# Kernel tuning notes

Hardware: AMD Instinct MI355X
Metric: run time of the kernel (lower is better)

The kernel has to match this reference:

```python
import jax, jax.numpy as jnp
import numpy as np

DIM = 2560; HEADS = 20; HEAD_DIM = 128
N_EXP = 4; TOP_K = 2; HID = 6912; SHID = 3584
B = 1; S = 2048
EPS = 1e-6


def setup_inputs():
    key = jax.random.key(0)
    ks = jax.random.split(key, 16)
    r = lambda i, shape, s=0.02: jax.random.normal(ks[i], shape, jnp.float32) * s
    # rope as [1,S,1,HD/2,2,2] rotation matrices: [[cos,-sin],[sin,cos]]
    ang = jax.random.uniform(ks[0], (1, S, 1, HEAD_DIM // 2), jnp.float32) * (2.0 * np.pi)
    c, s_ = jnp.cos(ang), jnp.sin(ang)
    rope = jnp.stack([jnp.stack([c, -s_], -1), jnp.stack([s_, c], -1)], -2)
    return dict(
        hidden_states=jax.random.normal(ks[1], (B, S, DIM), jnp.float32),
        temb=jax.random.normal(ks[2], (B, DIM), jnp.float32),
        rope=rope,
        adaln_w=r(3, (6 * DIM, DIM)), adaln_b=jnp.zeros((6 * DIM,), jnp.float32),
        qkv_w=r(4, (3 * DIM, DIM)), qkv_b=jnp.zeros((3 * DIM,), jnp.float32),
        qn_w=jnp.ones((DIM,), jnp.float32), kn_w=jnp.ones((DIM,), jnp.float32),
        out_w=r(5, (DIM, DIM)), out_b=jnp.zeros((DIM,), jnp.float32),
        gate_w=r(6, (N_EXP, DIM), 1.0 / DIM ** 0.5),
        ew1=r(7, (N_EXP, HID, DIM)), ew2=r(8, (N_EXP, DIM, HID)), ew3=r(9, (N_EXP, HID, DIM)),
        sw1=r(10, (SHID, DIM)), sw2=r(11, (DIM, SHID)), sw3=r(12, (SHID, DIM)),
    )


def _layernorm(x):  # elementwise_affine=False, eps=1e-6
    m = x.mean(-1, keepdims=True)
    v = ((x - m) ** 2).mean(-1, keepdims=True)
    return (x - m) * jax.lax.rsqrt(v + EPS)


def _rmsnorm(x, w):  # DistributedRMSNorm, tp_size=1
    return x * jax.lax.rsqrt((x ** 2).mean(-1, keepdims=True) + EPS) * w


def _apply_rope(x, rope):  # x:[B,S,H,D], rope:[1,S,1,D/2,2,2]
    b, s, h, d = x.shape
    x_ = x.reshape(b, s, h, d // 2, 1, 2)
    out = rope[..., 0] * x_[..., 0] + rope[..., 1] * x_[..., 1]  # [B,S,H,D/2,2]
    return out.reshape(b, s, h, d)


def _swiglu(x, w1, w2, w3):
    return (jax.nn.silu(x @ w1.T) * (x @ w3.T)) @ w2.T


def _forward(hidden_states, temb, rope, adaln_w, adaln_b, qkv_w, qkv_b, qn_w, kn_w,
             out_w, out_b, gate_w, ew1, ew2, ew3, sw1, sw2, sw3):
    b, s, d = hidden_states.shape
    # adaLN modulation: SiLU -> Linear -> [:, None] -> chunk(6)
    mod = (jax.nn.silu(temb) @ adaln_w.T + adaln_b)[:, None, :]
    shift_msa, scale_msa, gate_msa, shift_mlp, scale_mlp, gate_mlp = jnp.split(mod, 6, axis=-1)
    # --- attention ---
    nh = _layernorm(hidden_states) * (1.0 + scale_msa) + shift_msa
    qkv = nh @ qkv_w.T + qkv_b
    q, k, v = jnp.split(qkv, 3, axis=-1)  # each [B,S,inner_dim]
    q = _rmsnorm(q, qn_w)  # RMS over full inner_dim (all heads)
    k = _rmsnorm(k, kn_w)
    q = q.reshape(b, s, HEADS, HEAD_DIM)
    k = k.reshape(b, s, HEADS, HEAD_DIM)
    v = v.reshape(b, s, HEADS, HEAD_DIM)
    q = _apply_rope(q, rope)
    k = _apply_rope(k, rope)
    attn = jnp.einsum('bqhd,bkhd->bhqk', q, k) * (HEAD_DIM ** -0.5)
    attn = jax.nn.softmax(attn, axis=-1)
    o = jnp.einsum('bhqk,bkhd->bqhd', attn, v).reshape(b, s, HEADS * HEAD_DIM)
    o = o @ out_w.T + out_b
    hidden_states = gate_msa * o + hidden_states
    # --- MoE SwiGLU feed-forward ---
    nh = _layernorm(hidden_states) * (1.0 + scale_mlp) + shift_mlp
    x = nh.reshape(-1, d)  # [T,d]
    scores = jax.nn.softmax(x @ gate_w.T, axis=-1)  # [T,E]
    tw, ti = jax.lax.top_k(scores, TOP_K)  # norm_topk_prob=False
    t = x.shape[0]
    wdense = jnp.zeros((t, N_EXP), x.dtype).at[jnp.arange(t)[:, None], ti].set(tw)
    y = jnp.zeros_like(x)
    for e in range(N_EXP):  # fixed small expert count
        y = y + wdense[:, e:e + 1] * _swiglu(x, ew1[e], ew2[e], ew3[e])
    y = y.reshape(b, s, d) + _swiglu(nh, sw1, sw2, sw3)  # shared experts on identity
    return gate_mlp * y + hidden_states


def reference(hidden_states, temb, rope, adaln_w, adaln_b, qkv_w, qkv_b, qn_w, kn_w,
              out_w, out_b, gate_w, ew1, ew2, ew3, sw1, sw2, sw3):
    return _forward(hidden_states, temb, rope, adaln_w, adaln_b, qkv_w, qkv_b, qn_w, kn_w,
                    out_w, out_b, gate_w, ew1, ew2, ew3, sw1, sw2, sw3)
```

## Files before the change

### kernel.cpp

```cpp
#include <hip/hip_runtime.h>

#define DIM 2560
#define T_TOK 2048
#define NHEADS 20
#define HD 128
#define HID_E 6912
#define SHID_E 3584
#define MPAD 5120

typedef _Float16 f16x8 __attribute__((ext_vector_type(8)));
typedef float f32x4 __attribute__((ext_vector_type(4)));
typedef unsigned short u16x8 __attribute__((ext_vector_type(8)));

#define MFMA16(a, b, c) __builtin_amdgcn_mfma_f32_16x16x32_f16((a), (b), (c), 0, 0, 0)

__device__ inline unsigned short f2h(float f) {
  return __builtin_bit_cast(unsigned short, (_Float16)f);
}
__device__ inline float h2f(unsigned short u) {
  return (float)__builtin_bit_cast(_Float16, u);
}
__device__ inline float wave_sum(float v) {
#pragma unroll
  for (int off = 32; off > 0; off >>= 1) v += __shfl_down(v, off, 64);
  return v;
}
__device__ inline void gld16(const void* g, void* l) {
  __builtin_amdgcn_global_load_lds((const __attribute__((address_space(1))) void*)g,
                                   (__attribute__((address_space(3))) void*)l, 16, 0, 0);
}


__global__ __launch_bounds__(256) void silu_k(const float* __restrict__ t,
                                              float* __restrict__ ss) {
  int i = blockIdx.x * 256 + threadIdx.x;
  if (i < DIM) {
    float v = t[i];
    ss[i] = v / (1.f + expf(-v));
  }
}

__global__ __launch_bounds__(256) void cvt_f16(const float* __restrict__ in,
                                               unsigned short* __restrict__ outp, int n8) {
  const int stride = gridDim.x * 256;
  for (int i = blockIdx.x * 256 + threadIdx.x; i < n8; i += stride) {
    float4 a = *(const float4*)(in + (size_t)i * 8);
    float4 b = *(const float4*)(in + (size_t)i * 8 + 4);
    u16x8 u;
    u[0] = f2h(a.x); u[1] = f2h(a.y); u[2] = f2h(a.z); u[3] = f2h(a.w);
    u[4] = f2h(b.x); u[5] = f2h(b.y); u[6] = f2h(b.z); u[7] = f2h(b.w);
    *(u16x8*)&outp[(size_t)i * 8] = u;
  }
}

__global__ __launch_bounds__(256) void cvt_pair(const float* __restrict__ w1,
                                                const float* __restrict__ w3,
                                                unsigned short* __restrict__ outp) {
  const int j = blockIdx.x;
  const int g = j >> 5, r = j & 31;
  const float* src = (r < 16) ? (w1 + (size_t)(g * 16 + r) * DIM)
                              : (w3 + (size_t)(g * 16 + (r & 15)) * DIM);
  unsigned short* dst = outp + (size_t)j * DIM;
  for (int i = threadIdx.x; i < 320; i += 256) {
    float4 a = *(const float4*)(src + i * 8);
    float4 b = *(const float4*)(src + i * 8 + 4);
    u16x8 u;
    u[0] = f2h(a.x); u[1] = f2h(a.y); u[2] = f2h(a.z); u[3] = f2h(a.w);
    u[4] = f2h(b.x); u[5] = f2h(b.y); u[6] = f2h(b.z); u[7] = f2h(b.w);
    *(u16x8*)&dst[i * 8] = u;
  }
}

__global__ __launch_bounds__(256) void adaln_gemv(const float* __restrict__ ss,
                                                  const float* __restrict__ W,
                                                  const float* __restrict__ bias,
                                                  float* __restrict__ mod) {
  const int lane = threadIdx.x & 63;
  const int j = blockIdx.x * 4 + (threadIdx.x >> 6);
  const float* wr = W + (size_t)j * DIM;
  float p = 0.f;
  for (int i = lane; i < 640; i += 64) {
    float4 w = *(const float4*)(wr + i * 4);
    float4 x = *(const float4*)(ss + i * 4);
    p += w.x * x.x + w.y * x.y + w.z * x.z + w.w * x.w;
  }
  p = wave_sum(p);
  if (lane == 0) mod[j] = p + bias[j];
}

__global__ __launch_bounds__(256) void ln_mod(const float* __restrict__ x,
                                              const float* __restrict__ shift,
                                              const float* __restrict__ scale,
                                              unsigned short* __restrict__ outp) {
  __shared__ float rbuf[8];
  const int t = blockIdx.x, tid = threadIdx.x, lane = tid & 63, wid = tid >> 6;
  const float* xr = x + (size_t)t * DIM;
  float s = 0.f, sq = 0.f;
  for (int i = tid; i < 640; i += 256) {
    float4 v = *(const float4*)(xr + i * 4);
    s += v.x + v.y + v.z + v.w;
    sq += v.x * v.x + v.y * v.y + v.z * v.z + v.w * v.w;
  }
  s = wave_sum(s);
  sq = wave_sum(sq);
  if (lane == 0) {
    rbuf[wid] = s;
    rbuf[4 + wid] = sq;
  }
  __syncthreads();
  float S = rbuf[0] + rbuf[1] + rbuf[2] + rbuf[3];
  float SQ = rbuf[4] + rbuf[5] + rbuf[6] + rbuf[7];
  float mean = S * (1.f / DIM);
  float rs = rsqrtf(SQ * (1.f / DIM) - mean * mean + 1e-6f);
  for (int i = tid; i < 640; i += 256) {
    float4 v = *(const float4*)(xr + i * 4);
    float4 sc4 = *(const float4*)(scale + i * 4);
    float4 sh4 = *(const float4*)(shift + i * 4);
    ushort4 u;
    u.x = f2h((v.x - mean) * rs * (1.f + sc4.x) + sh4.x);
    u.y = f2h((v.y - mean) * rs * (1.f + sc4.y) + sh4.y);
    u.z = f2h((v.z - mean) * rs * (1.f + sc4.z) + sh4.z);
    u.w = f2h((v.w - mean) * rs * (1.f + sc4.w) + sh4.w);
    *(ushort4*)&outp[(size_t)t * DIM + i * 4] = u;
  }
}

__global__ __launch_bounds__(256) void rmsrope(const unsigned short* __restrict__ qkv,
                                               const float* __restrict__ qn,
                                               const float* __restrict__ kn,
                                               const float* __restrict__ rope,
                                               unsigned short* __restrict__ qh,
                                               unsigned short* __restrict__ kh) {
  __shared__ float rbuf[8];
  const int t = blockIdx.x, tid = threadIdx.x, lane = tid & 63, wid = tid >> 6;
  const unsigned short* row = qkv + (size_t)t * 7680;
  float sq = 0.f, sk = 0.f;
  for (int i = tid; i < 320; i += 256) {
    f16x8 qv = *(const f16x8*)(row + i * 8);
    f16x8 kv = *(const f16x8*)(row + DIM + i * 8);
#pragma unroll
    for (int j = 0; j < 8; ++j) {
      float q = (float)qv[j], k = (float)kv[j];
      sq += q * q;
      sk += k * k;
    }
  }
  sq = wave_sum(sq);
  sk = wave_sum(sk);
  if (lane == 0) {
    rbuf[wid] = sq;
    rbuf[4 + wid] = sk;
  }
  __syncthreads();
  float SQ = rbuf[0] + rbuf[1] + rbuf[2] + rbuf[3];
  float SK = rbuf[4] + rbuf[5] + rbuf[6] + rbuf[7];
  float rq = rsqrtf(SQ * (1.f / DIM) + 1e-6f) * 0.08838834764831845f;
  float rk = rsqrtf(SK * (1.f / DIM) + 1e-6f);
  for (int pp = tid; pp < 1280; pp += 256) {
    int c = pp * 2;
    float qe = h2f(row[c]) * rq * qn[c], qo = h2f(row[c + 1]) * rq * qn[c + 1];
    float ke = h2f(row[DIM + c]) * rk * kn[c], ko = h2f(row[DIM + c + 1]) * rk * kn[c + 1];
    float4 rr = *(const float4*)(rope + (size_t)t * 256 + (pp & 63) * 4);
    unsigned qp = (unsigned)f2h(rr.x * qe + rr.y * qo) |
                  ((unsigned)f2h(rr.z * qe + rr.w * qo) << 16);
    unsigned kp = (unsigned)f2h(rr.x * ke + rr.y * ko) |
                  ((unsigned)f2h(rr.z * ke + rr.w * ko) << 16);
    *(unsigned*)&qh[(size_t)t * DIM + c] = qp;
    *(unsigned*)&kh[(size_t)t * DIM + c] = kp;
  }
}

__global__ void transpose_v(const unsigned short* __restrict__ in,
                            unsigned short* __restrict__ outp) {
  __shared__ unsigned short tile[32][33];
  const int bx = blockIdx.x * 32;
  const int by = blockIdx.y * 32;
  const int tx = threadIdx.x, ty = threadIdx.y;
  for (int j = ty; j < 32; j += 8)
    tile[j][tx] = in[(size_t)(by + j) * 7680 + 5120 + bx + tx];
  __syncthreads();
  for (int j = ty; j < 32; j += 8)
    outp[(size_t)(bx + j) * T_TOK + by + tx] = tile[tx][j];
}

__global__ __launch_bounds__(256) void fattn(const unsigned short* __restrict__ qh,
                                             const unsigned short* __restrict__ kh,
                                             const unsigned short* __restrict__ vt,
                                             unsigned short* __restrict__ obuf) {
  __shared__ unsigned short sK[64 * 128];
  __shared__ unsigned short sV[128 * 64];
  __shared__ unsigned short sP[64 * 64];
  __shared__ float sRedM[4][64];
  __shared__ float sRedL[4][64];
  __shared__ float sM[64];
  __shared__ float sL[64];
  const int tid = threadIdx.x, lane = tid & 63, wv = tid >> 6;
  const int g = lane >> 4, fr = lane & 15;
  const int h = blockIdx.y;
  const int q0 = blockIdx.x * 64;

  {
    const int r = tid >> 2, qt = tid & 3;
    const unsigned short* gp = qh + (size_t)(q0 + r) * DIM + h * HD + qt * 32;
    uint4 v0 = ((const uint4*)gp)[0];
    uint4 v1 = ((const uint4*)gp)[1];
    uint4 v2 = ((const uint4*)gp)[2];
    uint4 v3 = ((const uint4*)gp)[3];
    unsigned short* dst = &sK[r * 128];
    const int cb = qt * 4, rs = r & 15;
    *(uint4*)&dst[((cb + 0) ^ rs) * 8] = v0;
    *(uint4*)&dst[((cb + 1) ^ rs) * 8] = v1;
    *(uint4*)&dst[((cb + 2) ^ rs) * 8] = v2;
    *(uint4*)&dst[((cb + 3) ^ rs) * 8] = v3;
  }
  __syncthreads();
  f16x8 qfrag[4][4];
#pragma unroll
  for (int ni = 0; ni < 4; ++ni) {
#pragma unroll
    for (int kt = 0; kt < 4; ++kt) {
      int r = ni * 16 + fr;
      qfrag[ni][kt] = *(const f16x8*)&sK[r * 128 + (((kt * 4 + g) ^ (r & 15)) << 3)];
    }
  }
  __syncthreads();

  f32x4 acco[4][2];
  f32x4 mprev[4];
  float mrun[4], lrun[4];
#pragma unroll
  for (int i = 0; i < 4; ++i) {
    acco[i][0] = (f32x4)0.f;
    acco[i][1] = (f32x4)0.f;
    mprev[i] = (f32x4)(-1e30f);
    mrun[i] = -1e30f;
    lrun[i] = 0.f;
  }

  for (int kt0 = 0; kt0 < T_TOK; kt0 += 64) {
    {
      const int r = tid >> 2, qt = tid & 3;
      const unsigned short* gp = kh + (size_t)(kt0 + r) * DIM + h * HD + qt * 32;
      uint4 v0 = ((const uint4*)gp)[0];
      uint4 v1 = ((const uint4*)gp)[1];
      uint4 v2 = ((const uint4*)gp)[2];
      uint4 v3 = ((const uint4*)gp)[3];
      unsigned short* dst = &sK[r * 128];
      const int cb = qt * 4, rs = r & 15;
      *(uint4*)&dst[((cb + 0) ^ rs) * 8] = v0;
      *(uint4*)&dst[((cb + 1) ^ rs) * 8] = v1;
      *(uint4*)&dst[((cb + 2) ^ rs) * 8] = v2;
      *(uint4*)&dst[((cb + 3) ^ rs) * 8] = v3;
      const int rv = tid >> 1, hf = tid & 1;
      const unsigned short* gv = vt + (size_t)(h * HD + rv) * T_TOK + kt0 + hf * 32;
      uint4 w0 = ((const uint4*)gv)[0];
      uint4 w1 = ((const uint4*)gv)[1];
      uint4 w2 = ((const uint4*)gv)[2];
      uint4 w3 = ((const uint4*)gv)[3];
      unsigned short* dv = &sV[rv * 64];
      const int cv = hf * 4, rvs = rv & 7;
      *(uint4*)&dv[((cv + 0) ^ rvs) * 8] = w0;
      *(uint4*)&dv[((cv + 1) ^ rvs) * 8] = w1;
      *(uint4*)&dv[((cv + 2) ^ rvs) * 8] = w2;
      *(uint4*)&dv[((cv + 3) ^ rvs) * 8] = w3;
    }
    __syncthreads();

    f32x4 accs[4] = {(f32x4)0.f, (f32x4)0.f, (f32x4)0.f, (f32x4)0.f};
#pragma unroll
    for (int kt = 0; kt < 4; ++kt) {
      int r = wv * 16 + fr;
      f16x8 ak = *(const f16x8*)&sK[r * 128 + (((kt * 4 + g) ^ (r & 15)) << 3)];
#pragma unroll
      for (int ni = 0; ni < 4; ++ni) accs[ni] = MFMA16(ak, qfrag[ni][kt], accs[ni]);
    }

    float pm[4];
#pragma unroll
    for (int ni = 0; ni < 4; ++ni) {
      float m = fmaxf(fmaxf(accs[ni][0], accs[ni][1]), fmaxf(accs[ni][2], accs[ni][3]));
      m = fmaxf(m, __shfl_xor(m, 16));
      m = fmaxf(m, __shfl_xor(m, 32));
      pm[ni] = m;
    }
    if (g == 0) {
#pragma unroll
      for (int ni = 0; ni < 4; ++ni) sRedM[wv][ni * 16 + fr] = pm[ni];
    }
    __syncthreads();
    float mnew[4];
#pragma unroll
    for (int ni = 0; ni < 4; ++ni) {
      int q = ni * 16 + fr;
      float mt = fmaxf(fmaxf(sRedM[0][q], sRedM[1][q]), fmaxf(sRedM[2][q], sRedM[3][q]));
      mnew[ni] = fmaxf(mrun[ni], mt);
    }
    float lsum[4];
#pragma unroll
    for (int ni = 0; ni < 4; ++ni) {
      float l0 = 0.f;
#pragma unroll
      for (int i = 0; i < 4; ++i) {
        float p = __expf(accs[ni][i] - mnew[ni]);
        accs[ni][i] = p;
        l0 += p;
      }
      l0 += __shfl_xor(l0, 16);
      l0 += __shfl_xor(l0, 32);
      lsum[ni] = l0;
    }
    if (g == 0) {
#pragma unroll
      for (int ni = 0; ni < 4; ++ni) sRedL[wv][ni * 16 + fr] = lsum[ni];
      if (wv == 0) {
#pragma unroll
        for (int ni = 0; ni < 4; ++ni) sM[ni * 16 + fr] = mnew[ni];
      }
    }
#pragma unroll
    for (int ni = 0; ni < 4; ++ni) {
      int q = ni * 16 + fr;
      unsigned p01 = (unsigned)f2h(accs[ni][0]) | ((unsigned)f2h(accs[ni][1]) << 16);
      unsigned p23 = (unsigned)f2h(accs[ni][2]) | ((unsigned)f2h(accs[ni][3]) << 16);
      uint2 pk;
      pk.x = p01;
      pk.y = p23;
      *(uint2*)&sP[q * 64 + ((((wv << 1) | (g >> 1)) ^ (q & 7)) << 3) + ((g & 1) << 2)] = pk;
    }
    __syncthreads();
#pragma unroll
    for (int ni = 0; ni < 4; ++ni) {
      int q = ni * 16 + fr;
      float lt = sRedL[0][q] + sRedL[1][q] + sRedL[2][q] + sRedL[3][q];
      lrun[ni] = lrun[ni] * __expf(mrun[ni] - mnew[ni]) + lt;
      mrun[ni] = mnew[ni];
    }

#pragma unroll
    for (int mi = 0; mi < 4; ++mi) {
      f32x4 mn = *(const f32x4*)&sM[mi * 16 + g * 4];
      f32x4 sc;
#pragma unroll
      for (int i = 0; i < 4; ++i) sc[i] = __expf(mprev[mi][i] - mn[i]);
      acco[mi][0] *= sc;
      acco[mi][1] *= sc;
      mprev[mi] = mn;
    }
#pragma unroll
    for (int ktp = 0; ktp < 2; ++ktp) {
      f16x8 bv[2];
#pragma unroll
      for (int nd = 0; nd < 2; ++nd) {
        int r = wv * 32 + nd * 16 + fr;
        bv[nd] = *(const f16x8*)&sV[r * 64 + (((ktp * 4 + g) ^ (r & 7)) << 3)];
      }
#pragma unroll
      for (int mi = 0; mi < 4; ++mi) {
        int r = mi * 16 + fr;
        f16x8 ap = *(const f16x8*)&sP[r * 64 + (((ktp * 4 + g) ^ (r & 7)) << 3)];
        acco[mi][0] = MFMA16(ap, bv[0], acco[mi][0]);
        acco[mi][1] = MFMA16(ap, bv[1], acco[mi][1]);
      }
    }
    __syncthreads();
  }

  if (wv == 0 && g == 0) {
#pragma unroll
    for (int ni = 0; ni < 4; ++ni) sL[ni * 16 + fr] = 1.f / lrun[ni];
  }
  __syncthreads();
#pragma unroll
  for (int mi = 0; mi < 4; ++mi) {
    f32x4 li = *(const f32x4*)&sL[mi * 16 + g * 4];
#pragma unroll
    for (int nd = 0; nd < 2; ++nd) {
#pragma unroll
      for (int i = 0; i < 4; ++i) {
        float o = acco[mi][nd][i] * li[i];
        obuf[(size_t)(q0 + mi * 16 + g * 4 + i) * DIM + h * HD + wv * 32 + nd * 16 + fr] =
            f2h(o);
      }
    }
  }
}

__global__ __launch_bounds__(256) void ln2_route(const float* __restrict__ x,
                                                 const float* __restrict__ shift,
                                                 const float* __restrict__ scale,
                                                 const float* __restrict__ gw,
                                                 unsigned short* __restrict__ nh2,
                                                 float* __restrict__ wd) {
  __shared__ float rbuf[8];
  __shared__ float gbuf[4][4];
  const int t = blockIdx.x, tid = threadIdx.x, lane = tid & 63, wid = tid >> 6;
  const float* xr = x + (size_t)t * DIM;
  float s = 0.f, sq = 0.f;
  for (int i = tid; i < 640; i += 256) {
    float4 v = *(const float4*)(xr + i * 4);
    s += v.x + v.y + v.z + v.w;
    sq += v.x * v.x + v.y * v.y + v.z * v.z + v.w * v.w;
  }
  s = wave_sum(s);
  sq = wave_sum(sq);
  if (lane == 0) {
    rbuf[wid] = s;
    rbuf[4 + wid] = sq;
  }
  __syncthreads();
  float S = rbuf[0] + rbuf[1] + rbuf[2] + rbuf[3];
  float SQ = rbuf[4] + rbuf[5] + rbuf[6] + rbuf[7];
  float mean = S * (1.f / DIM);
  float rs = rsqrtf(SQ * (1.f / DIM) - mean * mean + 1e-6f);
  float g0 = 0.f, g1 = 0.f, g2 = 0.f, g3 = 0.f;
  for (int i = tid; i < 640; i += 256) {
    float4 v = *(const float4*)(xr + i * 4);
    float4 sc4 = *(const float4*)(scale + i * 4);
    float4 sh4 = *(const float4*)(shift + i * 4);
    float y0 = (v.x - mean) * rs * (1.f + sc4.x) + sh4.x;
    float y1 = (v.y - mean) * rs * (1.f + sc4.y) + sh4.y;
    float y2 = (v.z - mean) * rs * (1.f + sc4.z) + sh4.z;
    float y3 = (v.w - mean) * rs * (1.f + sc4.w) + sh4.w;
    ushort4 u;
    u.x = f2h(y0); u.y = f2h(y1); u.z = f2h(y2); u.w = f2h(y3);
    *(ushort4*)&nh2[(size_t)t * DIM + i * 4] = u;
    float4 w0 = *(const float4*)(gw + i * 4);
    float4 w1 = *(const float4*)(gw + DIM + i * 4);
    float4 w2 = *(const float4*)(gw + 2 * DIM + i * 4);
    float4 w3 = *(const float4*)(gw + 3 * DIM + i * 4);
    g0 += y0 * w0.x + y1 * w0.y + y2 * w0.z + y3 * w0.w;
    g1 += y0 * w1.x + y1 * w1.y + y2 * w1.z + y3 * w1.w;
    g2 += y0 * w2.x + y1 * w2.y + y2 * w2.z + y3 * w2.w;
    g3 += y0 * w3.x + y1 * w3.y + y2 * w3.z + y3 * w3.w;
  }
  g0 = wave_sum(g0);
  g1 = wave_sum(g1);
  g2 = wave_sum(g2);
  g3 = wave_sum(g3);
  if (lane == 0) {
    gbuf[wid][0] = g0; gbuf[wid][1] = g1; gbuf[wid][2] = g2; gbuf[wid][3] = g3;
  }
  __syncthreads();
  if (tid == 0) {
    float l[4];
#pragma unroll
    for (int e = 0; e < 4; ++e) l[e] = gbuf[0][e] + gbuf[1][e] + gbuf[2][e] + gbuf[3][e];
    float mx = fmaxf(fmaxf(l[0], l[1]), fmaxf(l[2], l[3]));
    float ex[4], sum = 0.f;
#pragma unroll
    for (int e = 0; e < 4; ++e) { ex[e] = expf(l[e] - mx); sum += ex[e]; }
    float p[4];
#pragma unroll
    for (int e = 0; e < 4; ++e) p[e] = ex[e] / sum;
    int i1 = 0;
    for (int e = 1; e < 4; ++e)
      if (p[e] > p[i1]) i1 = e;
    int i2 = -1;
    for (int e = 0; e < 4; ++e) {
      if (e == i1) continue;
      if (i2 < 0 || p[e] > p[i2]) i2 = e;
    }
    float w[4] = {0.f, 0.f, 0.f, 0.f};
    w[i1] = p[i1];
    w[i2] = p[i2];
    *(float4*)&wd[(size_t)t * 4] = make_float4(w[0], w[1], w[2], w[3]);
  }
}

__global__ __launch_bounds__(256) void route_compact(const float* __restrict__ wd,
                                                     int* __restrict__ idx_all,
                                                     int* __restrict__ seg,
                                                     int* __restrict__ slotAB,
                                                     float* __restrict__ wAB) {
  __shared__ unsigned short c[256][4];
  __shared__ int offs[256][4];
  __shared__ int segs[5];
  const int t = threadIdx.x;
  for (int i = t; i < MPAD; i += 256) idx_all[i] = 0;
  unsigned char sel[8];
  float wv4[8][4];
  unsigned short lc[4] = {0, 0, 0, 0};
#pragma unroll
  for (int k = 0; k < 8; ++k) {
    int tok = t * 8 + k;
    float4 w = *(const float4*)&wd[(size_t)tok * 4];
    wv4[k][0] = w.x; wv4[k][1] = w.y; wv4[k][2] = w.z; wv4[k][3] = w.w;
    unsigned m = 0;
    if (w.x != 0.f) { m |= 1; lc[0]++; }
    if (w.y != 0.f) { m |= 2; lc[1]++; }
    if (w.z != 0.f) { m |= 4; lc[2]++; }
    if (w.w != 0.f) { m |= 8; lc[3]++; }
    sel[k] = (unsigned char)m;
  }
#pragma unroll
  for (int e = 0; e < 4; ++e) c[t][e] = lc[e];
  __syncthreads();
  if (t == 0) {
    int run[4] = {0, 0, 0, 0};
    for (int i = 0; i < 256; ++i) {
#pragma unroll
      for (int e = 0; e < 4; ++e) {
        offs[i][e] = run[e];
        run[e] += c[i][e];
      }
    }
    int s = 0;
    segs[0] = 0;
#pragma unroll
    for (int e = 0; e < 4; ++e) {
      s += (run[e] + 127) & ~127;
      segs[e + 1] = s;
    }
#pragma unroll
    for (int e = 0; e < 5; ++e) seg[e] = segs[e];
  }
  __syncthreads();
  int o[4];
#pragma unroll
  for (int e = 0; e < 4; ++e) o[e] = segs[e] + offs[t][e];
#pragma unroll
  for (int k = 0; k < 8; ++k) {
    int tok = t * 8 + k;
    unsigned m = sel[k];
    int sl[2] = {0, 0};
    float sw[2] = {0.f, 0.f};
    int ns = 0;
#pragma unroll
    for (int e = 0; e < 4; ++e) {
      if ((m >> e) & 1) {
        if (ns < 2) { sl[ns] = o[e]; sw[ns] = wv4[k][e]; }
        idx_all[o[e]++] = tok;
        ns++;
      }
    }
    if (ns == 1) { sl[1] = sl[0]; sw[1] = 0.f; }
    slotAB[tok * 2] = sl[0];
    slotAB[tok * 2 + 1] = sl[1];
    wAB[tok * 2] = sw[0];
    wAB[tok * 2 + 1] = sw[1];
  }
}

template <int EPI, int MODE>
__global__ __launch_bounds__(256) void gemm128(
    const unsigned short* __restrict__ A, const unsigned short* __restrict__ B,
    const float* __restrict__ bias, void* __restrict__ Cv,
    const float* __restrict__ aux0, const float* __restrict__ aux1,
    const int* __restrict__ idx, const int* __restrict__ seg,
    const int* __restrict__ slotAB, const float* __restrict__ wAB,
    const unsigned short* __restrict__ yc, int M, int N, int K) {
  __shared__ unsigned short smem[16384];
  const int tid = threadIdx.x;
  const int lane = tid & 63;
  const int wv = tid >> 6;
  const int nwg = gridDim.x;
  const int bid = blockIdx.x;
  const int swzb = (bid & 7) * (nwg >> 3) + (bid >> 3);
  const int gm = M >> 7;
  const int m0 = (swzb % gm) * 128, n0 = (swzb / gm) * 128;
  if (MODE != 0 && m0 >= seg[4]) return;

  const unsigned short* Bp = B;
  if constexpr (MODE != 0) {
    int e = 0;
#pragma unroll
    for (int i = 1; i < 4; ++i)
      if (m0 >= seg[i]) e = i;
    Bp = B + (size_t)e * N * K;
  }

  const int wm = (wv >> 1) * 64, wn = (wv & 1) * 64;
  const int fr = lane & 15, fc = lane >> 4;

  const int rl = lane >> 2, ch = lane & 3;
  const int R1 = wv * 16 + rl;
  const int R2 = 64 + R1;
  const int co1 = ((ch ^ ((R1 >> 1) & 3)) << 3);
  const int co2 = ((ch ^ ((R2 >> 1) & 3)) << 3);
  size_t ar1, ar2;
  if constexpr (MODE == 1) {
    ar1 = (size_t)idx[m0 + R1] * K;
    ar2 = (size_t)idx[m0 + R2] * K;
  } else {
    ar1 = (size_t)(m0 + R1) * K;
    ar2 = (size_t)(m0 + R2) * K;
  }
  const unsigned short* gA1 = A + ar1 + co1;
  const unsigned short* gA2 = A + ar2 + co2;
  const unsigned short* gB1 = Bp + (size_t)(n0 + R1) * K + co1;
  const unsigned short* gB2 = Bp + (size_t)(n0 + R2) * K + co2;
  const int lA1 = (wv * 16) * 32, lA2 = (64 + wv * 16) * 32;

  f32x4 acc[4][4];
#pragma unroll
  for (int i = 0; i < 4; ++i) {
#pragma unroll
    for (int j = 0; j < 4; ++j) acc[i][j] = (f32x4)0.f;
  }

  auto STAGE = [&](int buf, int kt) {
    unsigned short* base = smem + buf * 8192;
    gld16(gA1 + kt, base + lA1);
    gld16(gA2 + kt, base + lA2);
    gld16(gB1 + kt, base + 4096 + lA1);
    gld16(gB2 + kt, base + 4096 + lA2);
  };
  auto COMPUTE = [&](int buf) {
    const unsigned short* sA = smem + buf * 8192;
    const unsigned short* sB = sA + 4096;
    f16x8 a[4], b[4];
#pragma unroll
    for (int mi = 0; mi < 4; ++mi) {
      int r = wm + mi * 16 + fr;
      a[mi] = *(const f16x8*)&sA[r * 32 + ((fc ^ ((r >> 1) & 3)) << 3)];
    }
#pragma unroll
    for (int ni = 0; ni < 4; ++ni) {
      int r = wn + ni * 16 + fr;
      b[ni] = *(const f16x8*)&sB[r * 32 + ((fc ^ ((r >> 1) & 3)) << 3)];
    }
#pragma unroll
    for (int mi = 0; mi < 4; ++mi) {
#pragma unroll
      for (int ni = 0; ni < 4; ++ni) acc[mi][ni] = MFMA16(a[mi], b[ni], acc[mi][ni]);
    }
  };

  const int nk = K >> 5;
  STAGE(0, 0);
  __syncthreads();
  int cur = 0;
  for (int t = 1; t < nk; ++t) {
    STAGE(cur ^ 1, t << 5);
    COMPUTE(cur);
    __syncthreads();
    cur ^= 1;
  }
  COMPUTE(cur);

  if constexpr (EPI == 5) {
    unsigned short* Ch = (unsigned short*)Cv;
    const int Nh = N >> 1;
#pragma unroll
    for (int mi = 0; mi < 4; ++mi) {
#pragma unroll
      for (int p = 0; p < 2; ++p) {
        const int hcol = (((n0 + wn) >> 5) + p) * 16 + fr;
        const int mb = m0 + wm + mi * 16 + fc * 4;
#pragma unroll
        for (int i = 0; i < 4; ++i) {
          const int m = mb + i;
          float v1 = acc[mi][2 * p][i];
          float v3 = acc[mi][2 * p + 1][i];
          float y = v1 / (1.f + __expf(-v1)) * v3;
          Ch[(size_t)m * Nh + hcol] = f2h(y);
        }
      }
    }
    return;
  }
#pragma unroll
  for (int mi = 0; mi < 4; ++mi) {
#pragma unroll
    for (int ni = 0; ni < 4; ++ni) {
      const int n = n0 + wn + ni * 16 + fr;
      const int mb = m0 + wm + mi * 16 + fc * 4;
#pragma unroll
      for (int i = 0; i < 4; ++i) {
        const int m = mb + i;
        float v = acc[mi][ni][i];
        const size_t cidx = (size_t)m * N + n;
        if constexpr (EPI == 1) {
          ((float*)Cv)[cidx] = aux0[n] * (v + bias[n]) + aux1[cidx];
        } else if constexpr (EPI == 4) {
          if (bias) v += bias[n];
          ((unsigned short*)Cv)[cidx] = f2h(v);
        } else if constexpr (EPI == 6) {
          const int sA_ = slotAB[m * 2], sB_ = slotAB[m * 2 + 1];
          const float wA_ = wAB[m * 2], wB_ = wAB[m * 2 + 1];
          float vm = wA_ * h2f(yc[(size_t)sA_ * N + n]) + wB_ * h2f(yc[(size_t)sB_ * N + n]);
          ((float*)Cv)[cidx] = aux0[n] * (v + vm) + aux1[cidx];
        }
      }
    }
  }
}


extern "C" void kernel_launch(void* const* d_in, const int* in_sizes, int n_in,
                              void* d_out, int out_size, void* d_ws, size_t ws_size,
                              hipStream_t stream) {
  (void)in_sizes; (void)n_in; (void)out_size; (void)ws_size;
  const float* hs = (const float*)d_in[0];
  const float* temb = (const float*)d_in[1];
  const float* rope = (const float*)d_in[2];
  const float* adaw = (const float*)d_in[3];
  const float* adab = (const float*)d_in[4];
  const float* qkvw = (const float*)d_in[5];
  const float* qkvb = (const float*)d_in[6];
  const float* qnw = (const float*)d_in[7];
  const float* knw = (const float*)d_in[8];
  const float* outw = (const float*)d_in[9];
  const float* outb = (const float*)d_in[10];
  const float* gatew = (const float*)d_in[11];
  const float* ew1 = (const float*)d_in[12];
  const float* ew2 = (const float*)d_in[13];
  const float* ew3 = (const float*)d_in[14];
  const float* sw1 = (const float*)d_in[15];
  const float* sw2 = (const float*)d_in[16];
  const float* sw3 = (const float*)d_in[17];
  float* out = (float*)d_out;
  char* ws = (char*)d_ws;

  size_t off = 0;
  auto give = [&](size_t nbytes) {
    size_t r = off;
    off += (nbytes + 255) & ~(size_t)255;
    return r;
  };
  const size_t T = T_TOK, D = DIM;
  size_t o_mod = give(15360 * 4);
  size_t o_ss = give(D * 4);
  size_t o_wd = give(T * 4 * 4);
  size_t o_idx = give(MPAD * 4);
  size_t o_seg = give(8 * 4);
  size_t o_slot = give(T * 2 * 4);
  size_t o_wab = give(T * 2 * 4);
  size_t o_nh = give(T * D * 2);
  size_t o_qkvh = give(T * 7680 * 2);
  size_t o_qh = give(T * D * 2);
  size_t o_kh = give(T * D * 2);
  size_t o_vt = give(T * D * 2);
  size_t o_obf = give(T * D * 2);
  size_t o_h2 = give(T * D * 4);
  size_t o_yc = give((size_t)MPAD * D * 2);
  size_t o_hmid2 = give(T * SHID_E * 2);
  size_t o_qkvw = give((size_t)7680 * 2560 * 2);
  size_t o_outw = give((size_t)2560 * 2560 * 2);
  size_t o_ewA = give((size_t)4 * 2 * HID_E * 2560 * 2);
  size_t o_ew2 = give((size_t)4 * 2560 * HID_E * 2);
  size_t o_swA = give((size_t)2 * SHID_E * 2560 * 2);
  size_t o_sw2 = give((size_t)2560 * SHID_E * 2);

  float* mod = (float*)(ws + o_mod);
  float* ss = (float*)(ws + o_ss);
  float* wd = (float*)(ws + o_wd);
  int* idxb = (int*)(ws + o_idx);
  int* segp = (int*)(ws + o_seg);
  int* slotAB = (int*)(ws + o_slot);
  float* wAB = (float*)(ws + o_wab);
  unsigned short* nh_h = (unsigned short*)(ws + o_nh);
  unsigned short* qkvh = (unsigned short*)(ws + o_qkvh);
  unsigned short* qh = (unsigned short*)(ws + o_qh);
  unsigned short* kh = (unsigned short*)(ws + o_kh);
  unsigned short* vt = (unsigned short*)(ws + o_vt);
  unsigned short* obf = (unsigned short*)(ws + o_obf);
  float* h2 = (float*)(ws + o_h2);
  unsigned short* yc = (unsigned short*)(ws + o_yc);
  unsigned short* hmid2 = (unsigned short*)(ws + o_hmid2);
  unsigned short* qkvw_h = (unsigned short*)(ws + o_qkvw);
  unsigned short* outw_h = (unsigned short*)(ws + o_outw);
  unsigned short* ewA_h = (unsigned short*)(ws + o_ewA);
  unsigned short* ew2_h = (unsigned short*)(ws + o_ew2);
  unsigned short* swA_h = (unsigned short*)(ws + o_swA);
  unsigned short* sw2_h = (unsigned short*)(ws + o_sw2);
  unsigned short* nh2 = nh_h;
  unsigned short* hmid = qkvh;

  cvt_f16<<<2048, 256, 0, stream>>>(qkvw, qkvw_h, 7680 * 2560 / 8);
  cvt_f16<<<2048, 256, 0, stream>>>(outw, outw_h, 2560 * 2560 / 8);
  cvt_f16<<<2048, 256, 0, stream>>>(ew2, ew2_h, 4 * 2560 * HID_E / 8);
  cvt_f16<<<2048, 256, 0, stream>>>(sw2, sw2_h, 2560 * SHID_E / 8);
  for (int e = 0; e < 4; ++e) {
    cvt_pair<<<2 * HID_E, 256, 0, stream>>>(ew1 + (size_t)e * HID_E * DIM,
                                            ew3 + (size_t)e * HID_E * DIM,
                                            ewA_h + (size_t)e * 2 * HID_E * DIM);
  }
  cvt_pair<<<2 * SHID_E, 256, 0, stream>>>(sw1, sw3, swA_h);
  silu_k<<<10, 256, 0, stream>>>(temb, ss);
  adaln_gemv<<<3840, 256, 0, stream>>>(ss, adaw, adab, mod);
  ln_mod<<<T, 256, 0, stream>>>(hs, mod, mod + D, nh_h);
  gemm128<4, 0><<<16 * 60, 256, 0, stream>>>(nh_h, qkvw_h, qkvb, qkvh,
                                             nullptr, nullptr, nullptr, nullptr,
                                             nullptr, nullptr, nullptr, 2048, 7680, 2560);
  rmsrope<<<T, 256, 0, stream>>>(qkvh, qnw, knw, rope, qh, kh);
  transpose_v<<<dim3(80, 64), dim3(32, 8), 0, stream>>>(qkvh, vt);
  fattn<<<dim3(32, 20), 256, 0, stream>>>(qh, kh, vt, obf);
  gemm128<1, 0><<<16 * 20, 256, 0, stream>>>(obf, outw_h, outb, h2,
                                             mod + 2 * D, hs, nullptr, nullptr,
                                             nullptr, nullptr, nullptr, 2048, 2560, 2560);
  ln2_route<<<T, 256, 0, stream>>>(h2, mod + 3 * D, mod + 4 * D, gatew, nh2, wd);
  route_compact<<<1, 256, 0, stream>>>(wd, idxb, segp, slotAB, wAB);
  gemm128<5, 1><<<40 * 108, 256, 0, stream>>>(nh2, ewA_h, nullptr, hmid,
                                              nullptr, nullptr, idxb, segp,
                                              nullptr, nullptr, nullptr,
                                              MPAD, 2 * HID_E, 2560);
  gemm128<4, 2><<<40 * 20, 256, 0, stream>>>(hmid, ew2_h, nullptr, yc,
                                             nullptr, nullptr, nullptr, segp,
                                             nullptr, nullptr, nullptr,
                                             MPAD, 2560, 6912);
  gemm128<5, 0><<<16 * 56, 256, 0, stream>>>(nh2, swA_h, nullptr, hmid2,
                                             nullptr, nullptr, nullptr, nullptr,
                                             nullptr, nullptr, nullptr, 2048, 2 * SHID_E, 2560);
  gemm128<6, 0><<<16 * 20, 256, 0, stream>>>(hmid2, sw2_h, nullptr, out,
                                             mod + 5 * D, h2, nullptr, nullptr,
                                             slotAB, wAB, yc, 2048, 2560, 3584);
}
```

Baseline: 1.610 ms.

## Add 256x256-tile 512-thread GEMM kernel for QKV and expert up-projections

Introduces a gemm256 kernel with 256x256 output tiles, 8 waves, double-buffered LDS, interleaved global prefetch with MFMA groups, and s_setprio scheduling hints. It replaces the 128-tile GEMM for the QKV projection, the routed expert W1/W3 GEMM and the shared expert W1/W3 GEMM. Expert segment padding is raised to 256 rows to match the new tile. Larger tiles raise data reuse per block but cut the number of blocks (e.g. 240 for QKV), which risks poorer CU occupancy and more padded rows in the routed expert path.

```diff
diff --git a/kernel.cpp b/kernel.cpp
--- a/kernel.cpp
+++ b/kernel.cpp
@@ -508,7 +508,7 @@
     segs[0] = 0;
 #pragma unroll
     for (int e = 0; e < 4; ++e) {
-      s += (run[e] + 127) & ~127;
+      s += (run[e] + 255) & ~255;
       segs[e + 1] = s;
     }
 #pragma unroll
@@ -577,14 +577,8 @@
   const int R2 = 64 + R1;
   const int co1 = ((ch ^ ((R1 >> 1) & 3)) << 3);
   const int co2 = ((ch ^ ((R2 >> 1) & 3)) << 3);
-  size_t ar1, ar2;
-  if constexpr (MODE == 1) {
-    ar1 = (size_t)idx[m0 + R1] * K;
-    ar2 = (size_t)idx[m0 + R2] * K;
-  } else {
-    ar1 = (size_t)(m0 + R1) * K;
-    ar2 = (size_t)(m0 + R2) * K;
-  }
+  const size_t ar1 = (size_t)(m0 + R1) * K;
+  const size_t ar2 = (size_t)(m0 + R2) * K;
   const unsigned short* gA1 = A + ar1 + co1;
   const unsigned short* gA2 = A + ar2 + co2;
   const unsigned short* gB1 = Bp + (size_t)(n0 + R1) * K + co1;
@@ -638,27 +632,6 @@
   }
   COMPUTE(cur);
 
-  if constexpr (EPI == 5) {
-    unsigned short* Ch = (unsigned short*)Cv;
-    const int Nh = N >> 1;
-#pragma unroll
-    for (int mi = 0; mi < 4; ++mi) {
-#pragma unroll
-      for (int p = 0; p < 2; ++p) {
-        const int hcol = (((n0 + wn) >> 5) + p) * 16 + fr;
-        const int mb = m0 + wm + mi * 16 + fc * 4;
-#pragma unroll
-        for (int i = 0; i < 4; ++i) {
-          const int m = mb + i;
-          float v1 = acc[mi][2 * p][i];
-          float v3 = acc[mi][2 * p + 1][i];
-          float y = v1 / (1.f + __expf(-v1)) * v3;
-          Ch[(size_t)m * Nh + hcol] = f2h(y);
-        }
-      }
-    }
-    return;
-  }
 #pragma unroll
   for (int mi = 0; mi < 4; ++mi) {
 #pragma unroll
@@ -680,6 +653,197 @@
           const float wA_ = wAB[m * 2], wB_ = wAB[m * 2 + 1];
           float vm = wA_ * h2f(yc[(size_t)sA_ * N + n]) + wB_ * h2f(yc[(size_t)sB_ * N + n]);
           ((float*)Cv)[cidx] = aux0[n] * (v + vm) + aux1[cidx];
+        }
+      }
+    }
+  }
+}
+
+template <int EPI, int MODE>
+__global__ __launch_bounds__(512) void gemm256(
+    const unsigned short* __restrict__ A, const unsigned short* __restrict__ B,
+    const float* __restrict__ bias, void* __restrict__ Cv,
+    const int* __restrict__ idx, const int* __restrict__ seg,
+    int M, int N, int K) {
+  __shared__ unsigned short smem[32768];
+  const int tid = threadIdx.x;
+  const int lane = tid & 63;
+  const int wv = tid >> 6;
+  const int wr = wv >> 2;
+  const int wc = wv & 3;
+  const int fr = lane & 15, fc = lane >> 4;
+
+  const int nwg = gridDim.x;
+  const int bid = blockIdx.x;
+  const int swzb = (bid & 7) * (nwg >> 3) + (bid >> 3);
+  const int gm = M >> 8;
+  const int m0 = (swzb % gm) * 256, n0 = (swzb / gm) * 256;
+  if (MODE != 0 && m0 >= seg[4]) return;
+
+  const unsigned short* Bp = B;
+  if constexpr (MODE != 0) {
+    int e = 0;
+#pragma unroll
+    for (int i = 1; i < 4; ++i)
+      if (m0 >= seg[i]) e = i;
+    Bp = B + (size_t)e * N * K;
+  }
+
+  const int srow = (lane >> 2);
+  const int srcc = ((lane & 3) ^ ((lane >> 3) & 3)) << 3;
+  int mr0, mr1;
+  if constexpr (MODE == 1) {
+    mr0 = idx[m0 + wv * 16 + srow];
+    mr1 = idx[m0 + 128 + wv * 16 + srow];
+  } else {
+    mr0 = m0 + wv * 16 + srow;
+    mr1 = m0 + 128 + wv * 16 + srow;
+  }
+  const unsigned short* gA0 = A + (size_t)mr0 * K + srcc;
+  const unsigned short* gA1 = A + (size_t)mr1 * K + srcc;
+  const unsigned short* gB0 = Bp + (size_t)(n0 + wv * 16 + srow) * K + srcc;
+  const unsigned short* gB1 = Bp + (size_t)(n0 + 128 + wv * 16 + srow) * K + srcc;
+  const int lw = wv << 9;
+
+  const int sw = (fr >> 1) & 3;
+  const int fo = ((fc ^ sw) << 3);
+  const int aoff = (wr * 128 + fr) * 32 + fo;
+  const int boff = (wc * 64 + fr) * 32 + fo;
+
+  f32x4 acc[8][4];
+#pragma unroll
+  for (int i = 0; i < 8; ++i) {
+#pragma unroll
+    for (int j = 0; j < 4; ++j) acc[i][j] = (f32x4)0.f;
+  }
+
+  const int nk = K >> 5;
+  gld16(gA0, &smem[lw]);
+  gld16(gA1, &smem[4096 + lw]);
+  gld16(gB0, &smem[8192 + lw]);
+  gld16(gB1, &smem[12288 + lw]);
+  __syncthreads();
+
+  for (int t = 0; t < nk; ++t) {
+    const int cb = (t & 1) * 16384;
+    const int nb = cb ^ 16384;
+    const int kn = (t + 1) << 5;
+    const bool more = (t + 1) < nk;
+    const unsigned short* sA = smem + cb;
+    const unsigned short* sB = smem + cb + 8192;
+
+    f16x8 b0 = *(const f16x8*)&sB[boff];
+    f16x8 b1 = *(const f16x8*)&sB[boff + 512];
+    f16x8 b2 = *(const f16x8*)&sB[boff + 1024];
+    f16x8 b3 = *(const f16x8*)&sB[boff + 1536];
+    {
+      f16x8 a0 = *(const f16x8*)&sA[aoff];
+      f16x8 a1 = *(const f16x8*)&sA[aoff + 512];
+      if (more) {
+        gld16(gA0 + kn, &smem[nb + lw]);
+        gld16(gA1 + kn, &smem[nb + 4096 + lw]);
+      }
+      __builtin_amdgcn_sched_barrier(0);
+      __builtin_amdgcn_s_setprio(1);
+      acc[0][0] = MFMA16(a0, b0, acc[0][0]);
+      acc[0][1] = MFMA16(a0, b1, acc[0][1]);
+      acc[0][2] = MFMA16(a0, b2, acc[0][2]);
+      acc[0][3] = MFMA16(a0, b3, acc[0][3]);
+      acc[1][0] = MFMA16(a1, b0, acc[1][0]);
+      acc[1][1] = MFMA16(a1, b1, acc[1][1]);
+      acc[1][2] = MFMA16(a1, b2, acc[1][2]);
+      acc[1][3] = MFMA16(a1, b3, acc[1][3]);
+      __builtin_amdgcn_s_setprio(0);
+      __builtin_amdgcn_sched_barrier(0);
+    }
+    {
+      f16x8 a0 = *(const f16x8*)&sA[aoff + 1024];
+      f16x8 a1 = *(const f16x8*)&sA[aoff + 1536];
+      if (more) {
+        gld16(gB0 + kn, &smem[nb + 8192 + lw]);
+        gld16(gB1 + kn, &smem[nb + 12288 + lw]);
+      }
+      __builtin_amdgcn_sched_barrier(0);
+      __builtin_amdgcn_s_setprio(1);
+      acc[2][0] = MFMA16(a0, b0, acc[2][0]);
+      acc[2][1] = MFMA16(a0, b1, acc[2][1]);
+      acc[2][2] = MFMA16(a0, b2, acc[2][2]);
+      acc[2][3] = MFMA16(a0, b3, acc[2][3]);
+      acc[3][0] = MFMA16(a1, b0, acc[3][0]);
+      acc[3][1] = MFMA16(a1, b1, acc[3][1]);
+      acc[3][2] = MFMA16(a1, b2, acc[3][2]);
+      acc[3][3] = MFMA16(a1, b3, acc[3][3]);
+      __builtin_amdgcn_s_setprio(0);
+      __builtin_amdgcn_sched_barrier(0);
+    }
+    {
+      f16x8 a0 = *(const f16x8*)&sA[aoff + 2048];
+      f16x8 a1 = *(const f16x8*)&sA[aoff + 2560];
+      __builtin_amdgcn_sched_barrier(0);
+      __builtin_amdgcn_s_setprio(1);
+      acc[4][0] = MFMA16(a0, b0, acc[4][0]);
+      acc[4][1] = MFMA16(a0, b1, acc[4][1]);
+      acc[4][2] = MFMA16(a0, b2, acc[4][2]);
+      acc[4][3] = MFMA16(a0, b3, acc[4][3]);
+      acc[5][0] = MFMA16(a1, b0, acc[5][0]);
+      acc[5][1] = MFMA16(a1, b1, acc[5][1]);
+      acc[5][2] = MFMA16(a1, b2, acc[5][2]);
+      acc[5][3] = MFMA16(a1, b3, acc[5][3]);
+      __builtin_amdgcn_s_setprio(0);
+      __builtin_amdgcn_sched_barrier(0);
+    }
+    {
+      f16x8 a0 = *(const f16x8*)&sA[aoff + 3072];
+      f16x8 a1 = *(const f16x8*)&sA[aoff + 3584];
+      __builtin_amdgcn_sched_barrier(0);
+      __builtin_amdgcn_s_setprio(1);
+      acc[6][0] = MFMA16(a0, b0, acc[6][0]);
+      acc[6][1] = MFMA16(a0, b1, acc[6][1]);
+      acc[6][2] = MFMA16(a0, b2, acc[6][2]);
+      acc[6][3] = MFMA16(a0, b3, acc[6][3]);
+      acc[7][0] = MFMA16(a1, b0, acc[7][0]);
+      acc[7][1] = MFMA16(a1, b1, acc[7][1]);
+      acc[7][2] = MFMA16(a1, b2, acc[7][2]);
+      acc[7][3] = MFMA16(a1, b3, acc[7][3]);
+      __builtin_amdgcn_s_setprio(0);
+      __builtin_amdgcn_sched_barrier(0);
+    }
+    __syncthreads();
+  }
+
+  if constexpr (EPI == 5) {
+    unsigned short* Ch = (unsigned short*)Cv;
+    const int Nh = N >> 1;
+#pragma unroll
+    for (int mi = 0; mi < 8; ++mi) {
+#pragma unroll
+      for (int p = 0; p < 2; ++p) {
+        const int hcol = (((n0 + wc * 64) >> 5) + p) * 16 + fr;
+        const int mb = m0 + wr * 128 + mi * 16 + fc * 4;
+#pragma unroll
+        for (int i = 0; i < 4; ++i) {
+          const int m = mb + i;
+          float v1 = acc[mi][2 * p][i];
+          float v3 = acc[mi][2 * p + 1][i];
+          float y = v1 / (1.f + __expf(-v1)) * v3;
+          Ch[(size_t)m * Nh + hcol] = f2h(y);
+        }
+      }
+    }
+  } else {
+    unsigned short* Ch = (unsigned short*)Cv;
+#pragma unroll
+    for (int mi = 0; mi < 8; ++mi) {
+#pragma unroll
+      for (int ni = 0; ni < 4; ++ni) {
+        const int n = n0 + wc * 64 + ni * 16 + fr;
+        const int mb = m0 + wr * 128 + mi * 16 + fc * 4;
+#pragma unroll
+        for (int i = 0; i < 4; ++i) {
+          const int m = mb + i;
+          float v = acc[mi][ni][i];
+          if (bias) v += bias[n];
+          Ch[(size_t)m * N + n] = f2h(v);
         }
       }
     }
@@ -780,9 +944,8 @@
   silu_k<<<10, 256, 0, stream>>>(temb, ss);
   adaln_gemv<<<3840, 256, 0, stream>>>(ss, adaw, adab, mod);
   ln_mod<<<T, 256, 0, stream>>>(hs, mod, mod + D, nh_h);
-  gemm128<4, 0><<<16 * 60, 256, 0, stream>>>(nh_h, qkvw_h, qkvb, qkvh,
-                                             nullptr, nullptr, nullptr, nullptr,
-                                             nullptr, nullptr, nullptr, 2048, 7680, 2560);
+  gemm256<4, 0><<<240, 512, 0, stream>>>(nh_h, qkvw_h, qkvb, qkvh,
+                                         nullptr, nullptr, 2048, 7680, 2560);
   rmsrope<<<T, 256, 0, stream>>>(qkvh, qnw, knw, rope, qh, kh);
   transpose_v<<<dim3(80, 64), dim3(32, 8), 0, stream>>>(qkvh, vt);
   fattn<<<dim3(32, 20), 256, 0, stream>>>(qh, kh, vt, obf);
@@ -791,17 +954,14 @@
                                              nullptr, nullptr, nullptr, 2048, 2560, 2560);
   ln2_route<<<T, 256, 0, stream>>>(h2, mod + 3 * D, mod + 4 * D, gatew, nh2, wd);
   route_compact<<<1, 256, 0, stream>>>(wd, idxb, segp, slotAB, wAB);
-  gemm128<5, 1><<<40 * 108, 256, 0, stream>>>(nh2, ewA_h, nullptr, hmid,
-                                              nullptr, nullptr, idxb, segp,
-                                              nullptr, nullptr, nullptr,
-                                              MPAD, 2 * HID_E, 2560);
+  gemm256<5, 1><<<20 * 54, 512, 0, stream>>>(nh2, ewA_h, nullptr, hmid,
+                                             idxb, segp, MPAD, 2 * HID_E, 2560);
   gemm128<4, 2><<<40 * 20, 256, 0, stream>>>(hmid, ew2_h, nullptr, yc,
                                              nullptr, nullptr, nullptr, segp,
                                              nullptr, nullptr, nullptr,
                                              MPAD, 2560, 6912);
-  gemm128<5, 0><<<16 * 56, 256, 0, stream>>>(nh2, swA_h, nullptr, hmid2,
-                                             nullptr, nullptr, nullptr, nullptr,
-                                             nullptr, nullptr, nullptr, 2048, 2 * SHID_E, 2560);
+  gemm256<5, 0><<<8 * 28, 512, 0, stream>>>(nh2, swA_h, nullptr, hmid2,
+                                            nullptr, nullptr, 2048, 2 * SHID_E, 2560);
   gemm128<6, 0><<<16 * 20, 256, 0, stream>>>(hmid2, sw2_h, nullptr, out,
                                              mod + 5 * D, h2, nullptr, nullptr,
                                              slotAB, wAB, yc, 2048, 2560, 3584);
```

Result: faster. 1.487 ms (-7.6%).

## Add 256x256 tile GEMM kernel with 8 waves for QKV and MoE matmuls

Applied to the files above, without the earlier changes.

Introduces a new gemm256 kernel using 512 threads, 256x256 output tiles, K-step 64, double-buffered LDS with XOR swizzle, and a single barrier per iteration. It is used for the QKV projection, the expert up/down GEMMs and the shared-expert up GEMM. Expert segment padding grows to 256 rows to match the larger M tile. The larger tile raises arithmetic intensity and cuts global and LDS traffic per FLOP. The costs are 128KB of LDS, heavy register pressure from 32 accumulators per lane, fewer workgroups (240 for QKV), and more wasted padded rows.

```diff
diff --git a/kernel.cpp b/kernel.cpp
--- a/kernel.cpp
+++ b/kernel.cpp
@@ -508,7 +508,7 @@
     segs[0] = 0;
 #pragma unroll
     for (int e = 0; e < 4; ++e) {
-      s += (run[e] + 127) & ~127;
+      s += (run[e] + 255) & ~255;
       segs[e + 1] = s;
     }
 #pragma unroll
@@ -577,14 +577,8 @@
   const int R2 = 64 + R1;
   const int co1 = ((ch ^ ((R1 >> 1) & 3)) << 3);
   const int co2 = ((ch ^ ((R2 >> 1) & 3)) << 3);
-  size_t ar1, ar2;
-  if constexpr (MODE == 1) {
-    ar1 = (size_t)idx[m0 + R1] * K;
-    ar2 = (size_t)idx[m0 + R2] * K;
-  } else {
-    ar1 = (size_t)(m0 + R1) * K;
-    ar2 = (size_t)(m0 + R2) * K;
-  }
+  const size_t ar1 = (size_t)(m0 + R1) * K;
+  const size_t ar2 = (size_t)(m0 + R2) * K;
   const unsigned short* gA1 = A + ar1 + co1;
   const unsigned short* gA2 = A + ar2 + co2;
   const unsigned short* gB1 = Bp + (size_t)(n0 + R1) * K + co1;
@@ -638,27 +632,6 @@
   }
   COMPUTE(cur);
 
-  if constexpr (EPI == 5) {
-    unsigned short* Ch = (unsigned short*)Cv;
-    const int Nh = N >> 1;
-#pragma unroll
-    for (int mi = 0; mi < 4; ++mi) {
-#pragma unroll
-      for (int p = 0; p < 2; ++p) {
-        const int hcol = (((n0 + wn) >> 5) + p) * 16 + fr;
-        const int mb = m0 + wm + mi * 16 + fc * 4;
-#pragma unroll
-        for (int i = 0; i < 4; ++i) {
-          const int m = mb + i;
-          float v1 = acc[mi][2 * p][i];
-          float v3 = acc[mi][2 * p + 1][i];
-          float y = v1 / (1.f + __expf(-v1)) * v3;
-          Ch[(size_t)m * Nh + hcol] = f2h(y);
-        }
-      }
-    }
-    return;
-  }
 #pragma unroll
   for (int mi = 0; mi < 4; ++mi) {
 #pragma unroll
@@ -680,6 +653,149 @@
           const float wA_ = wAB[m * 2], wB_ = wAB[m * 2 + 1];
           float vm = wA_ * h2f(yc[(size_t)sA_ * N + n]) + wB_ * h2f(yc[(size_t)sB_ * N + n]);
           ((float*)Cv)[cidx] = aux0[n] * (v + vm) + aux1[cidx];
+        }
+      }
+    }
+  }
+}
+
+template <int EPI, int MODE>
+__global__ __launch_bounds__(512) void gemm256(
+    const unsigned short* __restrict__ A, const unsigned short* __restrict__ B,
+    const float* __restrict__ bias, void* __restrict__ Cv,
+    const int* __restrict__ idx, const int* __restrict__ seg,
+    int M, int N, int K) {
+  __shared__ unsigned short smem[65536];
+  const int tid = threadIdx.x;
+  const int lane = tid & 63;
+  const int wv = tid >> 6;
+  const int wr = wv >> 2;
+  const int wc = wv & 3;
+  const int fr = lane & 15, fc = lane >> 4;
+
+  const int nwg = gridDim.x;
+  const int bid = blockIdx.x;
+  const int swzb = (bid & 7) * (nwg >> 3) + (bid >> 3);
+  const int gm = M >> 8;
+  const int m0 = (swzb % gm) * 256, n0 = (swzb / gm) * 256;
+  if (MODE != 0 && m0 >= seg[4]) return;
+
+  const unsigned short* Bp = B;
+  if constexpr (MODE != 0) {
+    int e = 0;
+#pragma unroll
+    for (int i = 1; i < 4; ++i)
+      if (m0 >= seg[i]) e = i;
+    Bp = B + (size_t)e * N * K;
+  }
+
+  const int srl = lane >> 3;
+  const int scc = ((lane & 7) ^ srl) << 3;
+  const unsigned short* gA[4];
+  const unsigned short* gB[4];
+#pragma unroll
+  for (int s = 0; s < 4; ++s) {
+    int ar = m0 + wv * 32 + s * 8 + srl;
+    if constexpr (MODE == 1) ar = idx[ar];
+    gA[s] = A + (size_t)ar * K + scc;
+    gB[s] = Bp + (size_t)(n0 + wv * 32 + s * 8 + srl) * K + scc;
+  }
+  const int lws = wv * 2048 + lane * 8;
+
+  const int arow_ = wr * 128 + fr;
+  const int brow_ = wc * 64 + fr;
+  const int sl0 = (fc ^ (fr & 7)) << 3;
+  const int sl1 = ((4 + fc) ^ (fr & 7)) << 3;
+
+  f32x4 acc[8][4];
+#pragma unroll
+  for (int i = 0; i < 8; ++i) {
+#pragma unroll
+    for (int j = 0; j < 4; ++j) acc[i][j] = (f32x4)0.f;
+  }
+
+  auto STAGE = [&](int buf, int kt) {
+    unsigned short* ba = smem + buf * 32768;
+    unsigned short* bb = ba + 16384;
+#pragma unroll
+    for (int s = 0; s < 4; ++s) {
+      gld16(gA[s] + kt, ba + s * 512 + lws);
+      gld16(gB[s] + kt, bb + s * 512 + lws);
+    }
+  };
+
+  const int nk = K >> 6;
+  STAGE(0, 0);
+  for (int t = 0; t < nk; ++t) {
+    asm volatile("s_waitcnt vmcnt(0)" ::: "memory");
+    __builtin_amdgcn_s_barrier();
+    __builtin_amdgcn_sched_barrier(0);
+    const unsigned short* sA = smem + (t & 1) * 32768;
+    const unsigned short* sB = sA + 16384;
+    if (t + 1 < nk) STAGE((t + 1) & 1, (t + 1) << 6);
+    {
+      f16x8 b0 = *(const f16x8*)&sB[brow_ * 64 + sl0];
+      f16x8 b1 = *(const f16x8*)&sB[(brow_ + 16) * 64 + sl0];
+      f16x8 b2 = *(const f16x8*)&sB[(brow_ + 32) * 64 + sl0];
+      f16x8 b3 = *(const f16x8*)&sB[(brow_ + 48) * 64 + sl0];
+#pragma unroll
+      for (int mi = 0; mi < 8; ++mi) {
+        f16x8 a = *(const f16x8*)&sA[(arow_ + mi * 16) * 64 + sl0];
+        acc[mi][0] = MFMA16(a, b0, acc[mi][0]);
+        acc[mi][1] = MFMA16(a, b1, acc[mi][1]);
+        acc[mi][2] = MFMA16(a, b2, acc[mi][2]);
+        acc[mi][3] = MFMA16(a, b3, acc[mi][3]);
+      }
+    }
+    {
+      f16x8 b0 = *(const f16x8*)&sB[brow_ * 64 + sl1];
+      f16x8 b1 = *(const f16x8*)&sB[(brow_ + 16) * 64 + sl1];
+      f16x8 b2 = *(const f16x8*)&sB[(brow_ + 32) * 64 + sl1];
+      f16x8 b3 = *(const f16x8*)&sB[(brow_ + 48) * 64 + sl1];
+#pragma unroll
+      for (int mi = 0; mi < 8; ++mi) {
+        f16x8 a = *(const f16x8*)&sA[(arow_ + mi * 16) * 64 + sl1];
+        acc[mi][0] = MFMA16(a, b0, acc[mi][0]);
+        acc[mi][1] = MFMA16(a, b1, acc[mi][1]);
+        acc[mi][2] = MFMA16(a, b2, acc[mi][2]);
+        acc[mi][3] = MFMA16(a, b3, acc[mi][3]);
+      }
+    }
+  }
+
+  if constexpr (EPI == 5) {
+    unsigned short* Ch = (unsigned short*)Cv;
+    const int Nh = N >> 1;
+#pragma unroll
+    for (int mi = 0; mi < 8; ++mi) {
+#pragma unroll
+      for (int p = 0; p < 2; ++p) {
+        const int hcol = (((n0 + wc * 64) >> 5) + p) * 16 + fr;
+        const int mb = m0 + wr * 128 + mi * 16 + fc * 4;
+#pragma unroll
+        for (int i = 0; i < 4; ++i) {
+          const int m = mb + i;
+          float v1 = acc[mi][2 * p][i];
+          float v3 = acc[mi][2 * p + 1][i];
+          float y = v1 / (1.f + __expf(-v1)) * v3;
+          Ch[(size_t)m * Nh + hcol] = f2h(y);
+        }
+      }
+    }
+  } else {
+    unsigned short* Ch = (unsigned short*)Cv;
+#pragma unroll
+    for (int mi = 0; mi < 8; ++mi) {
+#pragma unroll
+      for (int ni = 0; ni < 4; ++ni) {
+        const int n = n0 + wc * 64 + ni * 16 + fr;
+        const int mb = m0 + wr * 128 + mi * 16 + fc * 4;
+#pragma unroll
+        for (int i = 0; i < 4; ++i) {
+          const int m = mb + i;
+          float v = acc[mi][ni][i];
+          if (bias) v += bias[n];
+          Ch[(size_t)m * N + n] = f2h(v);
         }
       }
     }
@@ -780,9 +896,8 @@
   silu_k<<<10, 256, 0, stream>>>(temb, ss);
   adaln_gemv<<<3840, 256, 0, stream>>>(ss, adaw, adab, mod);
   ln_mod<<<T, 256, 0, stream>>>(hs, mod, mod + D, nh_h);
-  gemm128<4, 0><<<16 * 60, 256, 0, stream>>>(nh_h, qkvw_h, qkvb, qkvh,
-                                             nullptr, nullptr, nullptr, nullptr,
-                                             nullptr, nullptr, nullptr, 2048, 7680, 2560);
+  gemm256<4, 0><<<240, 512, 0, stream>>>(nh_h, qkvw_h, qkvb, qkvh,
+                                         nullptr, nullptr, 2048, 7680, 2560);
   rmsrope<<<T, 256, 0, stream>>>(qkvh, qnw, knw, rope, qh, kh);
   transpose_v<<<dim3(80, 64), dim3(32, 8), 0, stream>>>(qkvh, vt);
   fattn<<<dim3(32, 20), 256, 0, stream>>>(qh, kh, vt, obf);
@@ -791,17 +906,12 @@
                                              nullptr, nullptr, nullptr, 2048, 2560, 2560);
   ln2_route<<<T, 256, 0, stream>>>(h2, mod + 3 * D, mod + 4 * D, gatew, nh2, wd);
   route_compact<<<1, 256, 0, stream>>>(wd, idxb, segp, slotAB, wAB);
-  gemm128<5, 1><<<40 * 108, 256, 0, stream>>>(nh2, ewA_h, nullptr, hmid,
-                                              nullptr, nullptr, idxb, segp,
-                                              nullptr, nullptr, nullptr,
-                                              MPAD, 2 * HID_E, 2560);
-  gemm128<4, 2><<<40 * 20, 256, 0, stream>>>(hmid, ew2_h, nullptr, yc,
-                                             nullptr, nullptr, nullptr, segp,
-                                             nullptr, nullptr, nullptr,
-                                             MPAD, 2560, 6912);
-  gemm128<5, 0><<<16 * 56, 256, 0, stream>>>(nh2, swA_h, nullptr, hmid2,
-                                             nullptr, nullptr, nullptr, nullptr,
-                                             nullptr, nullptr, nullptr, 2048, 2 * SHID_E, 2560);
+  gemm256<5, 1><<<20 * 54, 512, 0, stream>>>(nh2, ewA_h, nullptr, hmid,
+                                             idxb, segp, MPAD, 2 * HID_E, 2560);
+  gemm256<4, 2><<<20 * 10, 512, 0, stream>>>(hmid, ew2_h, nullptr, yc,
+                                             nullptr, segp, MPAD, 2560, 6912);
+  gemm256<5, 0><<<8 * 28, 512, 0, stream>>>(nh2, swA_h, nullptr, hmid2,
+                                            nullptr, nullptr, 2048, 2 * SHID_E, 2560);
   gemm128<6, 0><<<16 * 20, 256, 0, stream>>>(hmid2, sw2_h, nullptr, out,
                                              mod + 5 * D, h2, nullptr, nullptr,
                                              slotAB, wAB, yc, 2048, 2560, 3584);
```

After: 1.399 ms. 13.1% less time.
